# Kernel optimization log

Hardware: AMD Instinct MI355X
Metric: run time of the kernel (lower is better)

## Reference

```python
import jax, jax.numpy as jnp
import numpy as np

LAMBDA_MAX = 2.0  # standard re-scaled Laplacian assumption (DGL lambda_max=[2])
NUM_GRAPHS = 100


def _cheb(feat, src, dst, d_invsqrt, W, b):
    # DGL ChebConv: h = sum_i fc_i(X_i) + b, X_i = Chebyshev recursion on scaled Laplacian
    n = feat.shape[0]
    k = W.shape[0]
    re = 2.0 / LAMBDA_MAX

    def aggr(f):  # D^{-1/2} A D^{-1/2} f  via gather + segment_sum
        fh = f * d_invsqrt
        m = jax.ops.segment_sum(fh[src], dst, num_segments=n)
        return m * d_invsqrt

    X0 = feat
    h = X0 @ W[0]
    if k > 1:
        X1 = -re * aggr(X0) + X0 * (re - 1.0)
        h = h + X1 @ W[1]
        for i in range(2, k):
            Xi = -2.0 * re * aggr(X1) + X1 * (2.0 * (re - 1.0)) - X0
            h = h + Xi @ W[i]
            X0, X1 = X1, Xi
    return h + b


def _edgeconv(feat, src, dst, Wt, bt, Wp, bp):
    # DGL EdgeConv: out_i = max_{j->i} [theta(x_i - x_j) + phi(x_i)], 0 if no in-edges
    n = feat.shape[0]
    theta = (feat[dst] - feat[src]) @ Wt + bt           # [E, H]
    phi = feat @ Wp + bp                                # [N, H]
    msg = theta + phi[dst]                              # [E, H]
    agg = jax.ops.segment_max(msg, dst, num_segments=n)
    return jnp.where(jnp.isfinite(agg), agg, jnp.zeros((), feat.dtype))


def setup_inputs() -> dict:
    key = jax.random.key(0)
    ks = jax.random.split(key, 20)
    N, E, G = 100000, 1600000, NUM_GRAPHS
    IN, H, K = 16, 64, 3

    def lin(k, fan_in, shape):
        return jax.random.normal(k, shape, dtype=jnp.float32) * (1.0 / np.sqrt(fan_in))

    inp = {}
    inp["feat"] = jax.random.normal(ks[0], (N, IN), dtype=jnp.float32)
    inp["src"] = jax.random.randint(ks[1], (E,), 0, N)
    inp["dst"] = jax.random.randint(ks[2], (E,), 0, N)
    inp["graph_ids"] = jnp.sort(jax.random.randint(ks[3], (N,), 0, G))
    # ChebConv params: W [k, in, out], b [out]
    inp["W1"] = lin(ks[4], IN, (K, IN, H)); inp["b1"] = jnp.zeros((H,), jnp.float32)
    inp["W2"] = lin(ks[5], H, (K, H, H));   inp["b2"] = jnp.zeros((H,), jnp.float32)
    inp["W3"] = lin(ks[6], H, (K, H, H));   inp["b3"] = jnp.zeros((H,), jnp.float32)
    # EdgeConv params: theta + phi linears
    inp["Wt1"] = lin(ks[7], H, (H, H));  inp["bt1"] = jnp.zeros((H,), jnp.float32)
    inp["Wp1"] = lin(ks[8], H, (H, H));  inp["bp1"] = jnp.zeros((H,), jnp.float32)
    inp["Wt2"] = lin(ks[9], H, (H, H));  inp["bt2"] = jnp.zeros((H,), jnp.float32)
    inp["Wp2"] = lin(ks[10], H, (H, H)); inp["bp2"] = jnp.zeros((H,), jnp.float32)
    return inp


def reference(feat, src, dst, graph_ids, W1, b1, W2, b2, W3, b3,
              Wt1, bt1, Wp1, bp1, Wt2, bt2, Wp2, bp2):
    n = feat.shape[0]
    deg = jax.ops.segment_sum(jnp.ones((src.shape[0],), feat.dtype), dst, num_segments=n)
    d_invsqrt = (jnp.clip(deg, 1.0, None) ** -0.5)[:, None]  # [N, 1]

    h = jax.nn.relu(_cheb(feat, src, dst, d_invsqrt, W1, b1))
    h = jax.nn.relu(_edgeconv(h, src, dst, Wt1, bt1, Wp1, bp1))
    h = jax.nn.relu(_cheb(h, src, dst, d_invsqrt, W2, b2))
    h = jax.nn.relu(_edgeconv(h, src, dst, Wt2, bt2, Wp2, bp2))
    h = jax.nn.relu(_cheb(h, src, dst, d_invsqrt, W3, b3))

    # dgl.mean_nodes: per-graph mean pooling
    counts = jax.ops.segment_sum(jnp.ones((n,), h.dtype), graph_ids, num_segments=NUM_GRAPHS)
    hg = jax.ops.segment_sum(h, graph_ids, num_segments=NUM_GRAPHS)
    return hg / jnp.clip(counts, 1.0, None)[:, None]
```

## Files before the change

### kernel.cpp

```cpp
#include <hip/hip_runtime.h>
#include <hip/hip_bf16.h>
#include <math.h>

typedef __attribute__((ext_vector_type(8))) short short8;
typedef __attribute__((ext_vector_type(4))) float floatx4;

__device__ __forceinline__ unsigned short bfb(float x) {
    union { __hip_bfloat16 h; unsigned short u; } c;
    c.h = __float2bfloat16(x);
    return c.u;
}
__device__ __forceinline__ float bf2f(unsigned short u) {
    union { unsigned int i; float f; } c;
    c.i = ((unsigned int)u) << 16;
    return c.f;
}


__global__ __launch_bounds__(256) void k_bhist(const int* __restrict__ dst, int* __restrict__ bcnt, int E) {
    __shared__ int h[512];
    int t = threadIdx.x;
    for (int i = t; i < 512; i += 256) h[i] = 0;
    __syncthreads();
    int step = gridDim.x * 256;
    for (int i = blockIdx.x * 256 + t; i < E; i += step) atomicAdd(&h[dst[i] >> 8], 1);
    __syncthreads();
    for (int i = t; i < 512; i += 256) if (h[i]) atomicAdd(&bcnt[i], h[i]);
}

__global__ __launch_bounds__(512) void k_scanBkt(const int* __restrict__ bcnt, int* __restrict__ boff,
                                                 int* __restrict__ bcur, int nb, int E) {
    __shared__ int s[512];
    int t = threadIdx.x;
    int v = (t < nb) ? bcnt[t] : 0;
    s[t] = v;
    __syncthreads();
    for (int off = 1; off < 512; off <<= 1) {
        int x = (t >= off) ? s[t - off] : 0;
        __syncthreads();
        s[t] += x;
        __syncthreads();
    }
    if (t < nb) { boff[t] = s[t] - v; bcur[t] = s[t] - v; }
    if (t == 0) boff[nb] = E;
}

#define PCHUNK 8192

__global__ __launch_bounds__(256) void k_partA(const int* __restrict__ src, const int* __restrict__ dst,
                                               int* __restrict__ bcur, unsigned* __restrict__ ebuf, int E) {
    __shared__ int h[512];
    __shared__ int base[512];
    int t = threadIdx.x;
    for (int i = t; i < 512; i += 256) h[i] = 0;
    __syncthreads();
    int start = blockIdx.x * PCHUNK;
    int end = start + PCHUNK < E ? start + PCHUNK : E;
    for (int i = start + t; i < end; i += 256) atomicAdd(&h[dst[i] >> 8], 1);
    __syncthreads();
    for (int i = t; i < 512; i += 256) {
        int c = h[i];
        base[i] = c ? atomicAdd(&bcur[i], c) : 0;
        h[i] = 0;
    }
    __syncthreads();
    for (int i = start + t; i < end; i += 256) {
        int d = dst[i];
        int b = d >> 8;
        int r = atomicAdd(&h[b], 1);
        ebuf[base[b] + r] = ((unsigned)src[i] << 8) | (unsigned)(d & 255);
    }
}

__global__ __launch_bounds__(256) void k_finish(const unsigned* __restrict__ ebuf, const int* __restrict__ boff,
                                                int* __restrict__ row_off, float* __restrict__ dinv,
                                                int* __restrict__ csr, int N, int E) {
    __shared__ int h[256];
    __shared__ int sc[256];
    __shared__ int cur[256];
    int b = blockIdx.x, t = threadIdx.x;
    h[t] = 0;
    __syncthreads();
    int beg = boff[b], end = boff[b + 1];
    for (int e = beg + t; e < end; e += 256) atomicAdd(&h[ebuf[e] & 255], 1);
    __syncthreads();
    int v = h[t];
    sc[t] = v;
    __syncthreads();
    for (int off = 1; off < 256; off <<= 1) {
        int x = (t >= off) ? sc[t - off] : 0;
        __syncthreads();
        sc[t] += x;
        __syncthreads();
    }
    int node = (b << 8) + t;
    int excl = beg + sc[t] - v;
    if (node < N) {
        row_off[node] = excl;
        dinv[node] = rsqrtf((float)(v > 1 ? v : 1));
    }
    cur[t] = excl;
    if (b == 0 && t == 0) row_off[N] = E;
    __syncthreads();
    for (int e = beg + t; e < end; e += 256) {
        unsigned ed = ebuf[e];
        int pos = atomicAdd(&cur[ed & 255], 1);
        csr[pos] = (int)(ed >> 8);
    }
}


__global__ __launch_bounds__(256) void k_feat16(const float* __restrict__ feat, const float* __restrict__ dinv,
                                                unsigned short* __restrict__ featd, int total) {
    int i = blockIdx.x * 256 + threadIdx.x;
    if (i < total) featd[i] = bfb(feat[i] * dinv[i >> 4]);
}


__global__ __launch_bounds__(256) void k_aggr16(const unsigned short* __restrict__ Xd, const float* __restrict__ Z,
                                                const float* __restrict__ dinv,
                                                const int* __restrict__ row_off, const int* __restrict__ csr,
                                                float* __restrict__ out, unsigned short* __restrict__ outd,
                                                float alpha, float beta, int N) {
    const int D = 16;
    int t = blockIdx.x * blockDim.x + threadIdx.x;
    int node = t / D;
    int d = t % D;
    if (node >= N) return;
    int beg = row_off[node], end = row_off[node + 1];
    float a0 = 0.f, a1 = 0.f, a2 = 0.f, a3 = 0.f;
    int j = beg;
    for (; j + 3 < end; j += 4) {
        int s0 = csr[j], s1 = csr[j + 1], s2 = csr[j + 2], s3 = csr[j + 3];
        a0 += bf2f(Xd[s0 * D + d]);
        a1 += bf2f(Xd[s1 * D + d]);
        a2 += bf2f(Xd[s2 * D + d]);
        a3 += bf2f(Xd[s3 * D + d]);
    }
    for (; j < end; ++j) a0 += bf2f(Xd[csr[j] * D + d]);
    float acc = (a0 + a1) + (a2 + a3);
    float dn = dinv[node];
    float v = alpha * dn * acc;
    if (Z) v += beta * Z[node * D + d];
    out[node * D + d] = v;
    if (outd) outd[node * D + d] = bfb(v * dn);
}


__global__ __launch_bounds__(256) void k_aggr64(const unsigned short* __restrict__ Xd, const float* __restrict__ Z,
                                                const float* __restrict__ dinv,
                                                const int* __restrict__ row_off, const int* __restrict__ csr,
                                                unsigned short* __restrict__ outb, unsigned short* __restrict__ outd,
                                                float alpha, float beta, int N) {
    int node = blockIdx.x * 4 + (threadIdx.x >> 6);
    if (node >= N) return;
    int lane = threadIdx.x & 63;
    int g = lane >> 4;
    int c4 = (lane & 15) * 4;
    int beg = row_off[node], end = row_off[node + 1];
    int deg = end - beg;
    int myIdx = (lane < deg) ? csr[beg + lane] : 0;
    int dmain = deg < 64 ? deg : 64;
    float a0 = 0.f, a1 = 0.f, a2 = 0.f, a3 = 0.f;
    float b0 = 0.f, b1 = 0.f, b2 = 0.f, b3 = 0.f;
    int j = 0;
    for (; j + 15 < dmain; j += 16) {
        int sA = __shfl(myIdx, j + g);
        int sB = __shfl(myIdx, j + 4 + g);
        int sC = __shfl(myIdx, j + 8 + g);
        int sD = __shfl(myIdx, j + 12 + g);
        ushort4 xA = *(const ushort4*)&Xd[sA * 64 + c4];
        ushort4 xB = *(const ushort4*)&Xd[sB * 64 + c4];
        ushort4 xC = *(const ushort4*)&Xd[sC * 64 + c4];
        ushort4 xD = *(const ushort4*)&Xd[sD * 64 + c4];
        a0 += bf2f(xA.x); a1 += bf2f(xA.y); a2 += bf2f(xA.z); a3 += bf2f(xA.w);
        b0 += bf2f(xB.x); b1 += bf2f(xB.y); b2 += bf2f(xB.z); b3 += bf2f(xB.w);
        a0 += bf2f(xC.x); a1 += bf2f(xC.y); a2 += bf2f(xC.z); a3 += bf2f(xC.w);
        b0 += bf2f(xD.x); b1 += bf2f(xD.y); b2 += bf2f(xD.z); b3 += bf2f(xD.w);
    }
    for (; j + 7 < dmain; j += 8) {
        int sA = __shfl(myIdx, j + g);
        int sB = __shfl(myIdx, j + 4 + g);
        ushort4 xA = *(const ushort4*)&Xd[sA * 64 + c4];
        ushort4 xB = *(const ushort4*)&Xd[sB * 64 + c4];
        a0 += bf2f(xA.x); a1 += bf2f(xA.y); a2 += bf2f(xA.z); a3 += bf2f(xA.w);
        b0 += bf2f(xB.x); b1 += bf2f(xB.y); b2 += bf2f(xB.z); b3 += bf2f(xB.w);
    }
    for (; j < dmain; j += 4) {
        int idx = j + g;
        int s = __shfl(myIdx, idx < dmain ? idx : dmain - 1);
        ushort4 x = *(const ushort4*)&Xd[s * 64 + c4];
        if (idx < dmain) {
            a0 += bf2f(x.x); a1 += bf2f(x.y); a2 += bf2f(x.z); a3 += bf2f(x.w);
        }
    }
    for (int e = beg + 64; e < end; e += 4) {
        int idx = e + g;
        int s = csr[idx < end ? idx : end - 1];
        ushort4 x = *(const ushort4*)&Xd[s * 64 + c4];
        if (idx < end) {
            a0 += bf2f(x.x); a1 += bf2f(x.y); a2 += bf2f(x.z); a3 += bf2f(x.w);
        }
    }
    a0 += b0; a1 += b1; a2 += b2; a3 += b3;
    a0 += __shfl_xor(a0, 16); a0 += __shfl_xor(a0, 32);
    a1 += __shfl_xor(a1, 16); a1 += __shfl_xor(a1, 32);
    a2 += __shfl_xor(a2, 16); a2 += __shfl_xor(a2, 32);
    a3 += __shfl_xor(a3, 16); a3 += __shfl_xor(a3, 32);
    if (g == 0) {
        float dn = dinv[node];
        float v0 = alpha * dn * a0;
        float v1 = alpha * dn * a1;
        float v2 = alpha * dn * a2;
        float v3 = alpha * dn * a3;
        if (Z) {
            float4 zv = *(const float4*)&Z[(size_t)node * 64 + c4];
            v0 += beta * zv.x; v1 += beta * zv.y; v2 += beta * zv.z; v3 += beta * zv.w;
        }
        ushort4 ub = { bfb(v0), bfb(v1), bfb(v2), bfb(v3) };
        *(ushort4*)&outb[(size_t)node * 64 + c4] = ub;
        if (outd) {
            ushort4 u = { bfb(v0 * dn), bfb(v1 * dn), bfb(v2 * dn), bfb(v3 * dn) };
            *(ushort4*)&outd[(size_t)node * 64 + c4] = u;
        }
    }
}


template <int KDIM, bool BIN16, bool BOUT16>
__global__ __launch_bounds__(256) void k_cheb_m(const float* __restrict__ X0, const void* __restrict__ X1v,
                                                const void* __restrict__ X2v, const float* __restrict__ W,
                                                const float* __restrict__ b, void* __restrict__ outv, int N) {
    constexpr int KT = (KDIM == 16) ? 64 : 3 * KDIM;
    constexpr int SX = KT + 8;
    __shared__ unsigned short Xs[64 * SX];
    __shared__ unsigned short Ws[64 * SX];
    int t = threadIdx.x;

    {
        int sn = t & 63;
        int gn = blockIdx.x * 64 + sn; if (gn >= N) gn = N - 1;
        int k0 = (t >> 6) * (KDIM / 4);
#pragma unroll
        for (int i = 0; i < KDIM / 16; ++i) {
            float4 v = *(const float4*)&X0[(size_t)gn * KDIM + k0 + 4 * i];
            ushort4 u = { bfb(v.x), bfb(v.y), bfb(v.z), bfb(v.w) };
            *(ushort4*)&Xs[sn * SX + k0 + 4 * i] = u;
        }
        if constexpr (BIN16) {
            const unsigned short* X1 = (const unsigned short*)X1v;
            const unsigned short* X2 = (const unsigned short*)X2v;
#pragma unroll
            for (int i = 0; i < KDIM / 16; ++i) {
                *(ushort4*)&Xs[sn * SX + KDIM + k0 + 4 * i] =
                    *(const ushort4*)&X1[(size_t)gn * KDIM + k0 + 4 * i];
                *(ushort4*)&Xs[sn * SX + 2 * KDIM + k0 + 4 * i] =
                    *(const ushort4*)&X2[(size_t)gn * KDIM + k0 + 4 * i];
            }
        } else {
            const float* Xp[2] = { (const float*)X1v, (const float*)X2v };
#pragma unroll
            for (int a = 0; a < 2; ++a) {
#pragma unroll
                for (int i = 0; i < KDIM / 16; ++i) {
                    float4 v = *(const float4*)&Xp[a][(size_t)gn * KDIM + k0 + 4 * i];
                    ushort4 u = { bfb(v.x), bfb(v.y), bfb(v.z), bfb(v.w) };
                    *(ushort4*)&Xs[sn * SX + (a + 1) * KDIM + k0 + 4 * i] = u;
                }
            }
        }
        if (KDIM == 16) {
            int kp = 48 + (t >> 6) * 4;
            ushort4 z = { 0, 0, 0, 0 };
            *(ushort4*)&Xs[sn * SX + kp] = z;
        }
    }
    for (int idx = t; idx < 3 * KDIM * 64; idx += 256) {
        int a = idx / (KDIM * 64);
        int r = idx % (KDIM * 64);
        int k = r >> 6, n = r & 63;
        Ws[n * SX + a * KDIM + k] = bfb(W[idx]);
    }
    if (KDIM == 16) {
        for (int idx = t; idx < 1024; idx += 256) {
            int n = idx & 63, k = 48 + (idx >> 6);
            Ws[n * SX + k] = 0;
        }
    }
    __syncthreads();

    int wave = t >> 6, lane = t & 63;
    int fi = lane & 15, quad = lane >> 4;
    int arow = wave * 16 + fi;

    floatx4 acc0 = {0.f,0.f,0.f,0.f}, acc1 = {0.f,0.f,0.f,0.f}, acc2 = {0.f,0.f,0.f,0.f}, acc3 = {0.f,0.f,0.f,0.f};
#pragma unroll
    for (int ks = 0; ks < KT / 32; ++ks) {
        short8 af = *(const short8*)&Xs[arow * SX + ks * 32 + quad * 8];
        short8 b0 = *(const short8*)&Ws[(0 * 16 + fi) * SX + ks * 32 + quad * 8];
        short8 b1 = *(const short8*)&Ws[(1 * 16 + fi) * SX + ks * 32 + quad * 8];
        short8 b2 = *(const short8*)&Ws[(2 * 16 + fi) * SX + ks * 32 + quad * 8];
        short8 b3 = *(const short8*)&Ws[(3 * 16 + fi) * SX + ks * 32 + quad * 8];
        acc0 = __builtin_amdgcn_mfma_f32_16x16x32_bf16(af, b0, acc0, 0, 0, 0);
        acc1 = __builtin_amdgcn_mfma_f32_16x16x32_bf16(af, b1, acc1, 0, 0, 0);
        acc2 = __builtin_amdgcn_mfma_f32_16x16x32_bf16(af, b2, acc2, 0, 0, 0);
        acc3 = __builtin_amdgcn_mfma_f32_16x16x32_bf16(af, b3, acc3, 0, 0, 0);
    }

    int nbase = blockIdx.x * 64 + wave * 16 + quad * 4;
    floatx4 accs[4] = { acc0, acc1, acc2, acc3 };
#pragma unroll
    for (int nt = 0; nt < 4; ++nt) {
        int col = nt * 16 + fi;
        float bias = b[col];
#pragma unroll
        for (int reg = 0; reg < 4; ++reg) {
            int node = nbase + reg;
            if (node < N) {
                float r = fmaxf(accs[nt][reg] + bias, 0.f);
                if constexpr (BOUT16) {
                    ((unsigned short*)outv)[(size_t)node * 64 + col] = bfb(r);
                } else {
                    ((float*)outv)[(size_t)node * 64 + col] = r;
                }
            }
        }
    }
}


__global__ __launch_bounds__(256) void k_e1_m(const unsigned short* X, const float* __restrict__ Wt,
                                              const float* __restrict__ Wp, const float* __restrict__ bt,
                                              const float* __restrict__ bp,
                                              unsigned short* md, float* __restrict__ pbuf, int N) {
    constexpr int SX = 72;
    __shared__ unsigned short Xs[64 * SX];
    __shared__ unsigned short Ws[128 * SX];
    int t = threadIdx.x;

    {
        int sn = t & 63;
        int gn = blockIdx.x * 64 + sn; if (gn >= N) gn = N - 1;
        int k0 = (t >> 6) * 16;
#pragma unroll
        for (int i = 0; i < 2; ++i) {
            *(short8*)&Xs[sn * SX + k0 + 8 * i] = *(const short8*)&X[(size_t)gn * 64 + k0 + 8 * i];
        }
    }
    for (int idx = t; idx < 4096; idx += 256) {
        int k = idx >> 6, n = idx & 63;
        float wt = Wt[idx];
        Ws[n * SX + k] = bfb(wt);
        Ws[(64 + n) * SX + k] = bfb(wt + Wp[idx]);
    }
    __syncthreads();

    int wave = t >> 6, lane = t & 63;
    int fi = lane & 15, quad = lane >> 4;
    int arow = wave * 16 + fi;

    floatx4 acc[8];
#pragma unroll
    for (int i = 0; i < 8; ++i) acc[i] = (floatx4){0.f,0.f,0.f,0.f};
#pragma unroll
    for (int ks = 0; ks < 2; ++ks) {
        short8 af = *(const short8*)&Xs[arow * SX + ks * 32 + quad * 8];
#pragma unroll
        for (int nt = 0; nt < 8; ++nt) {
            short8 bf = *(const short8*)&Ws[(nt * 16 + fi) * SX + ks * 32 + quad * 8];
            acc[nt] = __builtin_amdgcn_mfma_f32_16x16x32_bf16(af, bf, acc[nt], 0, 0, 0);
        }
    }

    int nbase = blockIdx.x * 64 + wave * 16 + quad * 4;
#pragma unroll
    for (int nt = 0; nt < 8; ++nt) {
        int col = nt * 16 + fi;
        if (col < 64) {
#pragma unroll
            for (int reg = 0; reg < 4; ++reg) {
                int node = nbase + reg;
                if (node < N) md[(size_t)node * 64 + col] = bfb(acc[nt][reg]);
            }
        } else {
            int cc = col - 64;
            float bias = bt[cc] + bp[cc];
#pragma unroll
            for (int reg = 0; reg < 4; ++reg) {
                int node = nbase + reg;
                if (node < N) pbuf[(size_t)node * 64 + cc] = acc[nt][reg] + bias;
            }
        }
    }
}


__global__ __launch_bounds__(256) void k_e2_b(const unsigned short* __restrict__ md, const float* __restrict__ pbuf,
                                              const int* __restrict__ row_off, const int* __restrict__ csr,
                                              const float* __restrict__ dinv, float* __restrict__ out,
                                              unsigned short* __restrict__ outd, int N) {
    int node = blockIdx.x * 4 + (threadIdx.x >> 6);
    if (node >= N) return;
    int lane = threadIdx.x & 63;
    int g = lane >> 4;
    int c4 = (lane & 15) * 4;
    int beg = row_off[node], end = row_off[node + 1];
    int deg = end - beg;
    int myIdx = (lane < deg) ? csr[beg + lane] : 0;
    int dmain = deg < 64 ? deg : 64;
    float a0 = -INFINITY, a1 = -INFINITY, a2 = -INFINITY, a3 = -INFINITY;
    float b0 = -INFINITY, b1 = -INFINITY, b2 = -INFINITY, b3 = -INFINITY;
    int j = 0;
    for (; j + 15 < dmain; j += 16) {
        int sA = __shfl(myIdx, j + g);
        int sB = __shfl(myIdx, j + 4 + g);
        int sC = __shfl(myIdx, j + 8 + g);
        int sD = __shfl(myIdx, j + 12 + g);
        ushort4 xA = *(const ushort4*)&md[sA * 64 + c4];
        ushort4 xB = *(const ushort4*)&md[sB * 64 + c4];
        ushort4 xC = *(const ushort4*)&md[sC * 64 + c4];
        ushort4 xD = *(const ushort4*)&md[sD * 64 + c4];
        a0 = fmaxf(a0, -bf2f(xA.x)); a1 = fmaxf(a1, -bf2f(xA.y));
        a2 = fmaxf(a2, -bf2f(xA.z)); a3 = fmaxf(a3, -bf2f(xA.w));
        b0 = fmaxf(b0, -bf2f(xB.x)); b1 = fmaxf(b1, -bf2f(xB.y));
        b2 = fmaxf(b2, -bf2f(xB.z)); b3 = fmaxf(b3, -bf2f(xB.w));
        a0 = fmaxf(a0, -bf2f(xC.x)); a1 = fmaxf(a1, -bf2f(xC.y));
        a2 = fmaxf(a2, -bf2f(xC.z)); a3 = fmaxf(a3, -bf2f(xC.w));
        b0 = fmaxf(b0, -bf2f(xD.x)); b1 = fmaxf(b1, -bf2f(xD.y));
        b2 = fmaxf(b2, -bf2f(xD.z)); b3 = fmaxf(b3, -bf2f(xD.w));
    }
    for (; j + 7 < dmain; j += 8) {
        int sA = __shfl(myIdx, j + g);
        int sB = __shfl(myIdx, j + 4 + g);
        ushort4 xA = *(const ushort4*)&md[sA * 64 + c4];
        ushort4 xB = *(const ushort4*)&md[sB * 64 + c4];
        a0 = fmaxf(a0, -bf2f(xA.x)); a1 = fmaxf(a1, -bf2f(xA.y));
        a2 = fmaxf(a2, -bf2f(xA.z)); a3 = fmaxf(a3, -bf2f(xA.w));
        b0 = fmaxf(b0, -bf2f(xB.x)); b1 = fmaxf(b1, -bf2f(xB.y));
        b2 = fmaxf(b2, -bf2f(xB.z)); b3 = fmaxf(b3, -bf2f(xB.w));
    }
    for (; j < dmain; j += 4) {
        int idx = j + g;
        int s = __shfl(myIdx, idx < dmain ? idx : dmain - 1);
        ushort4 x = *(const ushort4*)&md[s * 64 + c4];
        if (idx < dmain) {
            a0 = fmaxf(a0, -bf2f(x.x)); a1 = fmaxf(a1, -bf2f(x.y));
            a2 = fmaxf(a2, -bf2f(x.z)); a3 = fmaxf(a3, -bf2f(x.w));
        }
    }
    for (int e = beg + 64; e < end; e += 4) {
        int idx = e + g;
        int s = csr[idx < end ? idx : end - 1];
        ushort4 x = *(const ushort4*)&md[s * 64 + c4];
        if (idx < end) {
            a0 = fmaxf(a0, -bf2f(x.x)); a1 = fmaxf(a1, -bf2f(x.y));
            a2 = fmaxf(a2, -bf2f(x.z)); a3 = fmaxf(a3, -bf2f(x.w));
        }
    }
    a0 = fmaxf(a0, b0); a1 = fmaxf(a1, b1); a2 = fmaxf(a2, b2); a3 = fmaxf(a3, b3);
    a0 = fmaxf(a0, __shfl_xor(a0, 16)); a0 = fmaxf(a0, __shfl_xor(a0, 32));
    a1 = fmaxf(a1, __shfl_xor(a1, 16)); a1 = fmaxf(a1, __shfl_xor(a1, 32));
    a2 = fmaxf(a2, __shfl_xor(a2, 16)); a2 = fmaxf(a2, __shfl_xor(a2, 32));
    a3 = fmaxf(a3, __shfl_xor(a3, 16)); a3 = fmaxf(a3, __shfl_xor(a3, 32));
    if (g == 0) {
        float r0 = 0.f, r1 = 0.f, r2 = 0.f, r3 = 0.f;
        if (end > beg) {
            float4 pv = *(const float4*)&pbuf[(size_t)node * 64 + c4];
            r0 = fmaxf(pv.x + a0, 0.f);
            r1 = fmaxf(pv.y + a1, 0.f);
            r2 = fmaxf(pv.z + a2, 0.f);
            r3 = fmaxf(pv.w + a3, 0.f);
        }
        float4 r = { r0, r1, r2, r3 };
        *(float4*)&out[(size_t)node * 64 + c4] = r;
        float dn = dinv[node];
        ushort4 u = { bfb(r0 * dn), bfb(r1 * dn), bfb(r2 * dn), bfb(r3 * dn) };
        *(ushort4*)&outd[(size_t)node * 64 + c4] = u;
    }
}


__global__ __launch_bounds__(256) void k_pool(const float* __restrict__ h, const int* __restrict__ gid,
                                              float* __restrict__ out, float* __restrict__ gcnt, int N) {
    const int CHUNK = 128;
    int wave = blockIdx.x * 4 + (threadIdx.x >> 6);
    int lane = threadIdx.x & 63;
    int beg = wave * CHUNK;
    if (beg >= N) return;
    int end = beg + CHUNK < N ? beg + CHUNK : N;
    int gcur = gid[beg];
    float acc = 0.f;
    int cnt = 0;
    for (int n = beg; n < end; ++n) {
        int g = gid[n];
        float v = h[n * 64 + lane];
        if (g != gcur) {
            atomicAdd(&out[gcur * 64 + lane], acc);
            if (lane == 0) atomicAdd(&gcnt[gcur], (float)cnt);
            gcur = g; acc = 0.f; cnt = 0;
        }
        acc += v;
        ++cnt;
    }
    atomicAdd(&out[gcur * 64 + lane], acc);
    if (lane == 0) atomicAdd(&gcnt[gcur], (float)cnt);
}

__global__ __launch_bounds__(256) void k_div(float* __restrict__ out, const float* __restrict__ gcnt, int total) {
    int i = blockIdx.x * blockDim.x + threadIdx.x;
    if (i < total) out[i] /= fmaxf(gcnt[i >> 6], 1.f);
}


extern "C" void kernel_launch(void* const* d_in, const int* in_sizes, int n_in,
                              void* d_out, int out_size, void* d_ws, size_t ws_size,
                              hipStream_t stream) {
    const float* feat = (const float*)d_in[0];
    const int* src = (const int*)d_in[1];
    const int* dst = (const int*)d_in[2];
    const int* gid = (const int*)d_in[3];
    const float* W1 = (const float*)d_in[4];  const float* b1 = (const float*)d_in[5];
    const float* W2 = (const float*)d_in[6];  const float* b2 = (const float*)d_in[7];
    const float* W3 = (const float*)d_in[8];  const float* b3 = (const float*)d_in[9];
    const float* Wt1 = (const float*)d_in[10]; const float* bt1 = (const float*)d_in[11];
    const float* Wp1 = (const float*)d_in[12]; const float* bp1 = (const float*)d_in[13];
    const float* Wt2 = (const float*)d_in[14]; const float* bt2 = (const float*)d_in[15];
    const float* Wp2 = (const float*)d_in[16]; const float* bp2 = (const float*)d_in[17];
    float* out = (float*)d_out;

    const int N = in_sizes[0] / 16;
    const int E = in_sizes[1];
    const int G = out_size / 64;
    const int nb = (N + 255) >> 8;

    char* p = (char*)d_ws;
    auto alloc = [&](size_t nbytes) {
        void* r = (void*)p;
        p += (nbytes + 255) & ~(size_t)255;
        return r;
    };
    int* row_off  = (int*)alloc((size_t)(N + 1) * 4);
    int* csr      = (int*)alloc((size_t)E * 4);
    int* bcnt     = (int*)alloc(512 * 4);
    int* boff     = (int*)alloc(513 * 4);
    int* bcur     = (int*)alloc(512 * 4);
    float* dinv   = (float*)alloc((size_t)N * 4);
    float* bufA   = (float*)alloc((size_t)N * 64 * 4);
    float* bufB   = (float*)alloc((size_t)N * 64 * 4);
    float* bufC   = (float*)alloc((size_t)N * 64 * 4);
    float* bufD   = (float*)alloc((size_t)N * 64 * 4);
    unsigned short* md = (unsigned short*)alloc((size_t)N * 64 * 2);
    float* gcnt   = (float*)alloc((size_t)G * 4);

    unsigned* ebuf = (unsigned*)bufA;
    unsigned short* hd = (unsigned short*)bufC;
    unsigned short* xd = (unsigned short*)bufC + (size_t)N * 64;
    unsigned short* hb = md;

    hipMemsetAsync(bcnt, 0, 512 * 4, stream);
    hipMemsetAsync(gcnt, 0, (size_t)G * 4, stream);
    hipMemsetAsync(d_out, 0, (size_t)out_size * 4, stream);

    const int nb16 = (N * 16 + 255) / 256;
    const int nbw = (N + 3) / 4;
    const int npool = ((N + 127) / 128 + 3) / 4;
    const int nbt = (N + 63) / 64;
    const int npart = (E + PCHUNK - 1) / PCHUNK;

    k_bhist<<<256, 256, 0, stream>>>(dst, bcnt, E);
    k_scanBkt<<<1, 512, 0, stream>>>(bcnt, boff, bcur, nb, E);
    k_partA<<<npart, 256, 0, stream>>>(src, dst, bcur, ebuf, E);
    k_finish<<<nb, 256, 0, stream>>>(ebuf, boff, row_off, dinv, csr, N, E);

    k_feat16<<<nb16, 256, 0, stream>>>(feat, dinv, hd, N * 16);
    k_aggr16<<<nb16, 256, 0, stream>>>(hd, nullptr, dinv, row_off, csr, bufA, xd, -1.f, 0.f, N);
    k_aggr16<<<nb16, 256, 0, stream>>>(xd, feat, dinv, row_off, csr, bufB, nullptr, -2.f, -1.f, N);
    k_cheb_m<16, false, true><<<nbt, 256, 0, stream>>>(feat, bufA, bufB, W1, b1, hb, N);

    k_e1_m<<<nbt, 256, 0, stream>>>(hb, Wt1, Wp1, bt1, bp1, md, bufB, N);
    k_e2_b<<<nbw, 256, 0, stream>>>(md, bufB, row_off, csr, dinv, bufD, hd, N);

    k_aggr64<<<nbw, 256, 0, stream>>>(hd, nullptr, dinv, row_off, csr, (unsigned short*)bufA, xd, -1.f, 0.f, N);
    k_aggr64<<<nbw, 256, 0, stream>>>(xd, bufD, dinv, row_off, csr, (unsigned short*)bufB, nullptr, -2.f, -1.f, N);
    k_cheb_m<64, true, true><<<nbt, 256, 0, stream>>>(bufD, bufA, bufB, W2, b2, hb, N);

    k_e1_m<<<nbt, 256, 0, stream>>>(hb, Wt2, Wp2, bt2, bp2, md, bufB, N);
    k_e2_b<<<nbw, 256, 0, stream>>>(md, bufB, row_off, csr, dinv, bufD, hd, N);

    k_aggr64<<<nbw, 256, 0, stream>>>(hd, nullptr, dinv, row_off, csr, (unsigned short*)bufA, xd, -1.f, 0.f, N);
    k_aggr64<<<nbw, 256, 0, stream>>>(xd, bufD, dinv, row_off, csr, (unsigned short*)bufB, nullptr, -2.f, -1.f, N);
    k_cheb_m<64, true, false><<<nbt, 256, 0, stream>>>(bufD, bufA, bufB, W3, b3, bufC, N);

    k_pool<<<npool, 256, 0, stream>>>(bufC, gid, out, gcnt, N);
    k_div<<<(out_size + 255) / 256, 256, 0, stream>>>(out, gcnt, out_size);
}
```

Measured before the change: 609.3 us.

## Use packed u16 ordered keys for edge max and wave-per-node aggr16

EdgeConv messages are stored as order-preserving 16-bit keys so the segment max uses packed unsigned 16-bit max instructions on raw loads instead of unpacking bf16 to float. The 16-wide Chebyshev aggregation is restructured to one wave per node with 8-byte vector gathers and shuffled neighbor offsets. Gather addresses are precomputed as byte offsets. The key encode and decode adds bit logic and changes how edge values round-trip through bf16.

```diff
diff --git a/kernel.cpp b/kernel.cpp
--- a/kernel.cpp
+++ b/kernel.cpp
@@ -14,6 +14,11 @@
     union { unsigned int i; float f; } c;
     c.i = ((unsigned int)u) << 16;
     return c.f;
+}
+__device__ __forceinline__ unsigned pkmaxu16(unsigned a, unsigned b) {
+    unsigned d;
+    asm("v_pk_max_u16 %0, %1, %2" : "=v"(d) : "v"(a), "v"(b));
+    return d;
 }
 
 
@@ -122,28 +127,60 @@
                                                 const int* __restrict__ row_off, const int* __restrict__ csr,
                                                 float* __restrict__ out, unsigned short* __restrict__ outd,
                                                 float alpha, float beta, int N) {
-    const int D = 16;
-    int t = blockIdx.x * blockDim.x + threadIdx.x;
-    int node = t / D;
-    int d = t % D;
+    int node = blockIdx.x * 4 + (threadIdx.x >> 6);
     if (node >= N) return;
+    int lane = threadIdx.x & 63;
+    int g = lane >> 2;
+    int co = (lane & 3) * 8;
     int beg = row_off[node], end = row_off[node + 1];
+    int deg = end - beg;
+    int myOff = ((lane < deg) ? csr[beg + lane] : 0) << 5;
+    int dmain = deg < 64 ? deg : 64;
     float a0 = 0.f, a1 = 0.f, a2 = 0.f, a3 = 0.f;
-    int j = beg;
-    for (; j + 3 < end; j += 4) {
-        int s0 = csr[j], s1 = csr[j + 1], s2 = csr[j + 2], s3 = csr[j + 3];
-        a0 += bf2f(Xd[s0 * D + d]);
-        a1 += bf2f(Xd[s1 * D + d]);
-        a2 += bf2f(Xd[s2 * D + d]);
-        a3 += bf2f(Xd[s3 * D + d]);
-    }
-    for (; j < end; ++j) a0 += bf2f(Xd[csr[j] * D + d]);
-    float acc = (a0 + a1) + (a2 + a3);
-    float dn = dinv[node];
-    float v = alpha * dn * acc;
-    if (Z) v += beta * Z[node * D + d];
-    out[node * D + d] = v;
-    if (outd) outd[node * D + d] = bfb(v * dn);
+    int j = 0;
+    for (; j + 15 < dmain; j += 16) {
+        int off = __shfl(myOff, j + g);
+        ushort4 x = *(const ushort4*)((const char*)Xd + off + co);
+        a0 += bf2f(x.x); a1 += bf2f(x.y); a2 += bf2f(x.z); a3 += bf2f(x.w);
+    }
+    if (j < dmain) {
+        int idx = j + g;
+        int off = __shfl(myOff, idx < dmain ? idx : dmain - 1);
+        ushort4 x = *(const ushort4*)((const char*)Xd + off + co);
+        if (idx < dmain) {
+            a0 += bf2f(x.x); a1 += bf2f(x.y); a2 += bf2f(x.z); a3 += bf2f(x.w);
+        }
+    }
+    for (int e = beg + 64; e < end; e += 16) {
+        int idx = e + g;
+        int s = csr[idx < end ? idx : end - 1];
+        ushort4 x = *(const ushort4*)((const char*)Xd + (s << 5) + co);
+        if (idx < end) {
+            a0 += bf2f(x.x); a1 += bf2f(x.y); a2 += bf2f(x.z); a3 += bf2f(x.w);
+        }
+    }
+    a0 += __shfl_xor(a0, 4); a0 += __shfl_xor(a0, 8); a0 += __shfl_xor(a0, 16); a0 += __shfl_xor(a0, 32);
+    a1 += __shfl_xor(a1, 4); a1 += __shfl_xor(a1, 8); a1 += __shfl_xor(a1, 16); a1 += __shfl_xor(a1, 32);
+    a2 += __shfl_xor(a2, 4); a2 += __shfl_xor(a2, 8); a2 += __shfl_xor(a2, 16); a2 += __shfl_xor(a2, 32);
+    a3 += __shfl_xor(a3, 4); a3 += __shfl_xor(a3, 8); a3 += __shfl_xor(a3, 16); a3 += __shfl_xor(a3, 32);
+    if (g == 0) {
+        int c4 = (lane & 3) * 4;
+        float dn = dinv[node];
+        float v0 = alpha * dn * a0;
+        float v1 = alpha * dn * a1;
+        float v2 = alpha * dn * a2;
+        float v3 = alpha * dn * a3;
+        if (Z) {
+            float4 zv = *(const float4*)&Z[(size_t)node * 16 + c4];
+            v0 += beta * zv.x; v1 += beta * zv.y; v2 += beta * zv.z; v3 += beta * zv.w;
+        }
+        float4 r = { v0, v1, v2, v3 };
+        *(float4*)&out[(size_t)node * 16 + c4] = r;
+        if (outd) {
+            ushort4 u = { bfb(v0 * dn), bfb(v1 * dn), bfb(v2 * dn), bfb(v3 * dn) };
+            *(ushort4*)&outd[(size_t)node * 16 + c4] = u;
+        }
+    }
 }
 
 
@@ -156,40 +193,40 @@
     if (node >= N) return;
     int lane = threadIdx.x & 63;
     int g = lane >> 4;
-    int c4 = (lane & 15) * 4;
+    int co = (lane & 15) * 8;
     int beg = row_off[node], end = row_off[node + 1];
     int deg = end - beg;
-    int myIdx = (lane < deg) ? csr[beg + lane] : 0;
+    int myOff = ((lane < deg) ? csr[beg + lane] : 0) << 7;
     int dmain = deg < 64 ? deg : 64;
     float a0 = 0.f, a1 = 0.f, a2 = 0.f, a3 = 0.f;
     float b0 = 0.f, b1 = 0.f, b2 = 0.f, b3 = 0.f;
     int j = 0;
     for (; j + 15 < dmain; j += 16) {
-        int sA = __shfl(myIdx, j + g);
-        int sB = __shfl(myIdx, j + 4 + g);
-        int sC = __shfl(myIdx, j + 8 + g);
-        int sD = __shfl(myIdx, j + 12 + g);
-        ushort4 xA = *(const ushort4*)&Xd[sA * 64 + c4];
-        ushort4 xB = *(const ushort4*)&Xd[sB * 64 + c4];
-        ushort4 xC = *(const ushort4*)&Xd[sC * 64 + c4];
-        ushort4 xD = *(const ushort4*)&Xd[sD * 64 + c4];
+        int oA = __shfl(myOff, j + g);
+        int oB = __shfl(myOff, j + 4 + g);
+        int oC = __shfl(myOff, j + 8 + g);
+        int oD = __shfl(myOff, j + 12 + g);
+        ushort4 xA = *(const ushort4*)((const char*)Xd + oA + co);
+        ushort4 xB = *(const ushort4*)((const char*)Xd + oB + co);
+        ushort4 xC = *(const ushort4*)((const char*)Xd + oC + co);
+        ushort4 xD = *(const ushort4*)((const char*)Xd + oD + co);
         a0 += bf2f(xA.x); a1 += bf2f(xA.y); a2 += bf2f(xA.z); a3 += bf2f(xA.w);
         b0 += bf2f(xB.x); b1 += bf2f(xB.y); b2 += bf2f(xB.z); b3 += bf2f(xB.w);
         a0 += bf2f(xC.x); a1 += bf2f(xC.y); a2 += bf2f(xC.z); a3 += bf2f(xC.w);
         b0 += bf2f(xD.x); b1 += bf2f(xD.y); b2 += bf2f(xD.z); b3 += bf2f(xD.w);
     }
     for (; j + 7 < dmain; j += 8) {
-        int sA = __shfl(myIdx, j + g);
-        int sB = __shfl(myIdx, j + 4 + g);
-        ushort4 xA = *(const ushort4*)&Xd[sA * 64 + c4];
-        ushort4 xB = *(const ushort4*)&Xd[sB * 64 + c4];
+        int oA = __shfl(myOff, j + g);
+        int oB = __shfl(myOff, j + 4 + g);
+        ushort4 xA = *(const ushort4*)((const char*)Xd + oA + co);
+        ushort4 xB = *(const ushort4*)((const char*)Xd + oB + co);
         a0 += bf2f(xA.x); a1 += bf2f(xA.y); a2 += bf2f(xA.z); a3 += bf2f(xA.w);
         b0 += bf2f(xB.x); b1 += bf2f(xB.y); b2 += bf2f(xB.z); b3 += bf2f(xB.w);
     }
     for (; j < dmain; j += 4) {
         int idx = j + g;
-        int s = __shfl(myIdx, idx < dmain ? idx : dmain - 1);
-        ushort4 x = *(const ushort4*)&Xd[s * 64 + c4];
+        int off = __shfl(myOff, idx < dmain ? idx : dmain - 1);
+        ushort4 x = *(const ushort4*)((const char*)Xd + off + co);
         if (idx < dmain) {
             a0 += bf2f(x.x); a1 += bf2f(x.y); a2 += bf2f(x.z); a3 += bf2f(x.w);
         }
@@ -197,7 +234,7 @@
     for (int e = beg + 64; e < end; e += 4) {
         int idx = e + g;
         int s = csr[idx < end ? idx : end - 1];
-        ushort4 x = *(const ushort4*)&Xd[s * 64 + c4];
+        ushort4 x = *(const ushort4*)((const char*)Xd + (s << 7) + co);
         if (idx < end) {
             a0 += bf2f(x.x); a1 += bf2f(x.y); a2 += bf2f(x.z); a3 += bf2f(x.w);
         }
@@ -208,6 +245,7 @@
     a2 += __shfl_xor(a2, 16); a2 += __shfl_xor(a2, 32);
     a3 += __shfl_xor(a3, 16); a3 += __shfl_xor(a3, 32);
     if (g == 0) {
+        int c4 = (lane & 15) * 4;
         float dn = dinv[node];
         float v0 = alpha * dn * a0;
         float v1 = alpha * dn * a1;
@@ -380,7 +418,11 @@
 #pragma unroll
             for (int reg = 0; reg < 4; ++reg) {
                 int node = nbase + reg;
-                if (node < N) md[(size_t)node * 64 + col] = bfb(acc[nt][reg]);
+                if (node < N) {
+                    unsigned u = (unsigned)bfb(acc[nt][reg]) ^ 0x8000u;
+                    unsigned key = (u & 0x8000u) ? (~u & 0xffffu) : (u | 0x8000u);
+                    md[(size_t)node * 64 + col] = (unsigned short)key;
+                }
             }
         } else {
             int cc = col - 64;
@@ -403,73 +445,70 @@
     if (node >= N) return;
     int lane = threadIdx.x & 63;
     int g = lane >> 4;
-    int c4 = (lane & 15) * 4;
+    int co = (lane & 15) * 8;
     int beg = row_off[node], end = row_off[node + 1];
     int deg = end - beg;
-    int myIdx = (lane < deg) ? csr[beg + lane] : 0;
+    int myOff = ((lane < deg) ? csr[beg + lane] : 0) << 7;
     int dmain = deg < 64 ? deg : 64;
-    float a0 = -INFINITY, a1 = -INFINITY, a2 = -INFINITY, a3 = -INFINITY;
-    float b0 = -INFINITY, b1 = -INFINITY, b2 = -INFINITY, b3 = -INFINITY;
+    unsigned kA0 = 0, kA1 = 0, kB0 = 0, kB1 = 0;
     int j = 0;
     for (; j + 15 < dmain; j += 16) {
-        int sA = __shfl(myIdx, j + g);
-        int sB = __shfl(myIdx, j + 4 + g);
-        int sC = __shfl(myIdx, j + 8 + g);
-        int sD = __shfl(myIdx, j + 12 + g);
-        ushort4 xA = *(const ushort4*)&md[sA * 64 + c4];
-        ushort4 xB = *(const ushort4*)&md[sB * 64 + c4];
-        ushort4 xC = *(const ushort4*)&md[sC * 64 + c4];
-        ushort4 xD = *(const ushort4*)&md[sD * 64 + c4];
-        a0 = fmaxf(a0, -bf2f(xA.x)); a1 = fmaxf(a1, -bf2f(xA.y));
-        a2 = fmaxf(a2, -bf2f(xA.z)); a3 = fmaxf(a3, -bf2f(xA.w));
-        b0 = fmaxf(b0, -bf2f(xB.x)); b1 = fmaxf(b1, -bf2f(xB.y));
-        b2 = fmaxf(b2, -bf2f(xB.z)); b3 = fmaxf(b3, -bf2f(xB.w));
-        a0 = fmaxf(a0, -bf2f(xC.x)); a1 = fmaxf(a1, -bf2f(xC.y));
-        a2 = fmaxf(a2, -bf2f(xC.z)); a3 = fmaxf(a3, -bf2f(xC.w));
-        b0 = fmaxf(b0, -bf2f(xD.x)); b1 = fmaxf(b1, -bf2f(xD.y));
-        b2 = fmaxf(b2, -bf2f(xD.z)); b3 = fmaxf(b3, -bf2f(xD.w));
+        int oA = __shfl(myOff, j + g);
+        int oB = __shfl(myOff, j + 4 + g);
+        int oC = __shfl(myOff, j + 8 + g);
+        int oD = __shfl(myOff, j + 12 + g);
+        uint2 xA = *(const uint2*)((const char*)md + oA + co);
+        uint2 xB = *(const uint2*)((const char*)md + oB + co);
+        uint2 xC = *(const uint2*)((const char*)md + oC + co);
+        uint2 xD = *(const uint2*)((const char*)md + oD + co);
+        kA0 = pkmaxu16(kA0, xA.x); kA1 = pkmaxu16(kA1, xA.y);
+        kB0 = pkmaxu16(kB0, xB.x); kB1 = pkmaxu16(kB1, xB.y);
+        kA0 = pkmaxu16(kA0, xC.x); kA1 = pkmaxu16(kA1, xC.y);
+        kB0 = pkmaxu16(kB0, xD.x); kB1 = pkmaxu16(kB1, xD.y);
     }
     for (; j + 7 < dmain; j += 8) {
-        int sA = __shfl(myIdx, j + g);
-        int sB = __shfl(myIdx, j + 4 + g);
-        ushort4 xA = *(const ushort4*)&md[sA * 64 + c4];
-        ushort4 xB = *(const ushort4*)&md[sB * 64 + c4];
-        a0 = fmaxf(a0, -bf2f(xA.x)); a1 = fmaxf(a1, -bf2f(xA.y));
-        a2 = fmaxf(a2, -bf2f(xA.z)); a3 = fmaxf(a3, -bf2f(xA.w));
-        b0 = fmaxf(b0, -bf2f(xB.x)); b1 = fmaxf(b1, -bf2f(xB.y));
-        b2 = fmaxf(b2, -bf2f(xB.z)); b3 = fmaxf(b3, -bf2f(xB.w));
+        int oA = __shfl(myOff, j + g);
+        int oB = __shfl(myOff, j + 4 + g);
+        uint2 xA = *(const uint2*)((const char*)md + oA + co);
+        uint2 xB = *(const uint2*)((const char*)md + oB + co);
+        kA0 = pkmaxu16(kA0, xA.x); kA1 = pkmaxu16(kA1, xA.y);
+        kB0 = pkmaxu16(kB0, xB.x); kB1 = pkmaxu16(kB1, xB.y);
     }
     for (; j < dmain; j += 4) {
         int idx = j + g;
-        int s = __shfl(myIdx, idx < dmain ? idx : dmain - 1);
-        ushort4 x = *(const ushort4*)&md[s * 64 + c4];
-        if (idx < dmain) {
-            a0 = fmaxf(a0, -bf2f(x.x)); a1 = fmaxf(a1, -bf2f(x.y));
-            a2 = fmaxf(a2, -bf2f(x.z)); a3 = fmaxf(a3, -bf2f(x.w));
-        }
+        int off = __shfl(myOff, idx < dmain ? idx : dmain - 1);
+        uint2 x = *(const uint2*)((const char*)md + off + co);
+        kA0 = pkmaxu16(kA0, idx < dmain ? x.x : 0u);
+        kA1 = pkmaxu16(kA1, idx < dmain ? x.y : 0u);
     }
     for (int e = beg + 64; e < end; e += 4) {
         int idx = e + g;
         int s = csr[idx < end ? idx : end - 1];
-        ushort4 x = *(const ushort4*)&md[s * 64 + c4];
-        if (idx < end) {
-            a0 = fmaxf(a0, -bf2f(x.x)); a1 = fmaxf(a1, -bf2f(x.y));
-            a2 = fmaxf(a2, -bf2f(x.z)); a3 = fmaxf(a3, -bf2f(x.w));
-        }
-    }
-    a0 = fmaxf(a0, b0); a1 = fmaxf(a1, b1); a2 = fmaxf(a2, b2); a3 = fmaxf(a3, b3);
-    a0 = fmaxf(a0, __shfl_xor(a0, 16)); a0 = fmaxf(a0, __shfl_xor(a0, 32));
-    a1 = fmaxf(a1, __shfl_xor(a1, 16)); a1 = fmaxf(a1, __shfl_xor(a1, 32));
-    a2 = fmaxf(a2, __shfl_xor(a2, 16)); a2 = fmaxf(a2, __shfl_xor(a2, 32));
-    a3 = fmaxf(a3, __shfl_xor(a3, 16)); a3 = fmaxf(a3, __shfl_xor(a3, 32));
+        uint2 x = *(const uint2*)((const char*)md + (s << 7) + co);
+        kA0 = pkmaxu16(kA0, idx < end ? x.x : 0u);
+        kA1 = pkmaxu16(kA1, idx < end ? x.y : 0u);
+    }
+    kA0 = pkmaxu16(kA0, kB0); kA1 = pkmaxu16(kA1, kB1);
+    kA0 = pkmaxu16(kA0, __shfl_xor((int)kA0, 16)); kA0 = pkmaxu16(kA0, __shfl_xor((int)kA0, 32));
+    kA1 = pkmaxu16(kA1, __shfl_xor((int)kA1, 16)); kA1 = pkmaxu16(kA1, __shfl_xor((int)kA1, 32));
     if (g == 0) {
+        int c4 = (lane & 15) * 4;
+        unsigned short ks[4] = { (unsigned short)(kA0 & 0xffff), (unsigned short)(kA0 >> 16),
+                                 (unsigned short)(kA1 & 0xffff), (unsigned short)(kA1 >> 16) };
+        float a[4];
+#pragma unroll
+        for (int i = 0; i < 4; ++i) {
+            unsigned k = ks[i];
+            unsigned short tt = (k & 0x8000u) ? (unsigned short)(k & 0x7fffu) : (unsigned short)(~k & 0xffffu);
+            a[i] = bf2f(tt);
+        }
         float r0 = 0.f, r1 = 0.f, r2 = 0.f, r3 = 0.f;
         if (end > beg) {
             float4 pv = *(const float4*)&pbuf[(size_t)node * 64 + c4];
-            r0 = fmaxf(pv.x + a0, 0.f);
-            r1 = fmaxf(pv.y + a1, 0.f);
-            r2 = fmaxf(pv.z + a2, 0.f);
-            r3 = fmaxf(pv.w + a3, 0.f);
+            r0 = fmaxf(pv.x + a[0], 0.f);
+            r1 = fmaxf(pv.y + a[1], 0.f);
+            r2 = fmaxf(pv.z + a[2], 0.f);
+            r3 = fmaxf(pv.w + a[3], 0.f);
         }
         float4 r = { r0, r1, r2, r3 };
         *(float4*)&out[(size_t)node * 64 + c4] = r;
@@ -573,8 +612,8 @@
     k_finish<<<nb, 256, 0, stream>>>(ebuf, boff, row_off, dinv, csr, N, E);
 
     k_feat16<<<nb16, 256, 0, stream>>>(feat, dinv, hd, N * 16);
-    k_aggr16<<<nb16, 256, 0, stream>>>(hd, nullptr, dinv, row_off, csr, bufA, xd, -1.f, 0.f, N);
-    k_aggr16<<<nb16, 256, 0, stream>>>(xd, feat, dinv, row_off, csr, bufB, nullptr, -2.f, -1.f, N);
+    k_aggr16<<<nbw, 256, 0, stream>>>(hd, nullptr, dinv, row_off, csr, bufA, xd, -1.f, 0.f, N);
+    k_aggr16<<<nbw, 256, 0, stream>>>(xd, feat, dinv, row_off, csr, bufB, nullptr, -2.f, -1.f, N);
     k_cheb_m<16, false, true><<<nbt, 256, 0, stream>>>(feat, bufA, bufB, W1, b1, hb, N);
 
     k_e1_m<<<nbt, 256, 0, stream>>>(hb, Wt1, Wp1, bt1, bp1, md, bufB, N);
```

Measured after the change: 621.3 us. Within noise of the previous version (+2.0%).
